# Kernel tuning notes

Measured on AMD Instinct MI355X. Metric: run time of the kernel, lower is better.

## Reference

```python
import jax, jax.numpy as jnp
import numpy as np

B, S, D, H = 32, 8192, 256, 256


def setup_inputs() -> dict:
    key = jax.random.key(0)
    ks = jax.random.split(key, 8)
    # start token: module uses np.random.seed(42); np.random.random([B,1,D])
    rng = np.random.RandomState(42)
    start_token = jnp.asarray(rng.random_sample((B, 1, D)).astype(np.float32))
    s = 0.05  # weight init scale
    return {
        "encoder_output": jax.random.normal(ks[0], (B, S, D), jnp.float32),
        "h0": jax.random.normal(ks[1], (B, H), jnp.float32),
        "c0": jax.random.normal(ks[2], (B, H), jnp.float32),
        "start_token": start_token,
        # Keras LSTM params: kernel [D,4H], recurrent_kernel [H,4H], bias [4H]; gate order i,f,c,o
        "W_k": jax.random.normal(ks[3], (D, 4 * H), jnp.float32) * s,
        "W_r": jax.random.normal(ks[4], (H, 4 * H), jnp.float32) * s,
        "b_lstm": jnp.zeros((4 * H,), jnp.float32),
        # encoder_weight Dense(H), decode_weight Dense(H), v Dense(1)
        "W_e": jax.random.normal(ks[5], (D, H), jnp.float32) * s,
        "b_e": jnp.zeros((H,), jnp.float32),
        "W_d": jax.random.normal(ks[6], (H, H), jnp.float32) * s,
        "b_d": jnp.zeros((H,), jnp.float32),
        "v_w": jax.random.normal(ks[7], (H, 1), jnp.float32) * s,
        "v_b": jnp.zeros((1,), jnp.float32),
    }


def reference(encoder_output, h0, c0, start_token, W_k, W_r, b_lstm,
              W_e, b_e, W_d, b_d, v_w, v_b):
    # --- one Keras-LSTM step on the start token (seq_len = 1) ---
    x = start_token[:, 0, :]                      # [B, D]
    z = x @ W_k + h0 @ W_r + b_lstm               # [B, 4H]
    i, f, g, o = jnp.split(z, 4, axis=-1)         # Keras gate order i,f,c,o
    c = jax.nn.sigmoid(f) * c0 + jax.nn.sigmoid(i) * jnp.tanh(g)
    h = jax.nn.sigmoid(o) * jnp.tanh(c)           # [B, H] decoder output
    # --- Bahdanau additive attention (vectorized form of the double loop) ---
    dec_proj = h @ W_d + b_d                      # [B, H]
    enc_proj = encoder_output @ W_e + b_e         # [B, S, H]
    # tanh(enc_proj + dec_proj) projected to scalar by v
    scores = jnp.tanh(enc_proj + dec_proj[:, None, :]) @ v_w  # [B, S, 1]
    scores = scores[..., 0] + v_b                 # [B, S]
    return jax.nn.softmax(scores, axis=-1)
```

## Files before the change

kernel.cpp:

```cpp
#include <hip/hip_runtime.h>
#include <hip/hip_bf16.h>
#include <stdint.h>

#define B 32
#define S 8192
#define D 256
#define H 256

typedef __attribute__((ext_vector_type(8))) short bf16x8;
typedef __attribute__((ext_vector_type(4))) float f32x4;

__device__ inline unsigned short f2bf(float f) {
  unsigned u = __float_as_uint(f);
  unsigned r = (u + 0x7FFFu + ((u >> 16) & 1u)) >> 16;
  return (unsigned short)r;
}

__device__ inline unsigned pk2bf(float a, float b) {
  __hip_bfloat162 h = __float22bfloat162_rn(make_float2(a, b));
  unsigned u;
  __builtin_memcpy(&u, &h, 4);
  return u;
}

__device__ inline bf16x8 pack8(float4 a, float4 b) {
  union { unsigned u[4]; bf16x8 v; } c;
  c.u[0] = pk2bf(a.x, a.y);
  c.u[1] = pk2bf(a.z, a.w);
  c.u[2] = pk2bf(b.x, b.y);
  c.u[3] = pk2bf(b.z, b.w);
  return c.v;
}

__device__ inline float fast_tanh(float x) {
  float e = __expf(2.0f * x);
  return 1.0f - 2.0f * __builtin_amdgcn_rcpf(1.0f + e);
}

__global__ __launch_bounds__(1024) void prep_kernel(
    const float* __restrict__ h0, const float* __restrict__ c0,
    const float* __restrict__ start_token, const float* __restrict__ W_k,
    const float* __restrict__ W_r, const float* __restrict__ b_lstm,
    const float* __restrict__ W_e, const float* __restrict__ W_d,
    const float* __restrict__ b_d,
    unsigned short* __restrict__ Wfrag, float* __restrict__ dec) {
  int blk = blockIdx.x;
  int tid = threadIdx.x;

  __shared__ float xs[D], hs[H], zs[4 * H], hv[H], dpp[4][H];

  if (blk < 64) {
    int gid = blk * 1024 + tid;
    int j = gid & 7;
    int lane = (gid >> 3) & 63;
    int kt = (gid >> 9) & 7;
    int nt = gid >> 12;
    int n = nt * 16 + (lane & 15);
    int k = kt * 32 + (lane >> 4) * 8 + j;
    Wfrag[gid] = f2bf(W_e[k * H + n]);
  } else {
    int b = blk - 64;
    if (tid < D) xs[tid] = start_token[b * D + tid];
    else if (tid < 2 * D) hs[tid - D] = h0[b * H + (tid - D)];
    __syncthreads();
    {
      int jj = tid;
      float a0 = 0.f, a1 = 0.f, a2 = 0.f, a3 = 0.f;
      #pragma unroll 8
      for (int d = 0; d < D; d += 4) {
        a0 += xs[d + 0] * W_k[(d + 0) * 1024 + jj];
        a1 += xs[d + 1] * W_k[(d + 1) * 1024 + jj];
        a2 += xs[d + 2] * W_k[(d + 2) * 1024 + jj];
        a3 += xs[d + 3] * W_k[(d + 3) * 1024 + jj];
      }
      #pragma unroll 8
      for (int h = 0; h < H; h += 4) {
        a0 += hs[h + 0] * W_r[(h + 0) * 1024 + jj];
        a1 += hs[h + 1] * W_r[(h + 1) * 1024 + jj];
        a2 += hs[h + 2] * W_r[(h + 2) * 1024 + jj];
        a3 += hs[h + 3] * W_r[(h + 3) * 1024 + jj];
      }
      zs[jj] = b_lstm[jj] + ((a0 + a1) + (a2 + a3));
    }
    __syncthreads();
    if (tid < H) {
      float zi = zs[tid], zf = zs[H + tid], zg = zs[2 * H + tid], zo = zs[3 * H + tid];
      float si = 1.0f / (1.0f + expf(-zi));
      float sf = 1.0f / (1.0f + expf(-zf));
      float so = 1.0f / (1.0f + expf(-zo));
      float c = sf * c0[b * H + tid] + si * tanhf(zg);
      hv[tid] = so * tanhf(c);
    }
    __syncthreads();
    {
      int hcol = tid & (H - 1);
      int q = tid >> 8;
      float a = 0.f;
      #pragma unroll 8
      for (int k = q * 64; k < q * 64 + 64; ++k) a += hv[k] * W_d[k * H + hcol];
      dpp[q][hcol] = a;
    }
    __syncthreads();
    if (tid < H)
      dec[b * H + tid] = dpp[0][tid] + dpp[1][tid] + dpp[2][tid] + dpp[3][tid] + b_d[tid];
  }
}

__global__ __launch_bounds__(256, 2) void attn_kernel(
    const float* __restrict__ enc, const unsigned short* __restrict__ Wfrag,
    const float* __restrict__ dec, const float* __restrict__ b_e,
    const float* __restrict__ v_w, float* __restrict__ scores) {
  __shared__ float part_sh[2][64];

  int tid = threadIdx.x;
  int b = blockIdx.x >> 7;
  int st = blockIdx.x & 127;
  long row0 = (long)b * S + st * 64;

  int wave = tid >> 6, lane = tid & 63;
  int ml = lane & 15, kg = lane >> 4;
  int wr = wave >> 1, wc = wave & 1;

  const float* arow0 = enc + (row0 + wr * 32 + ml) * (long)D + kg * 8;
  const float* arow1 = arow0 + 16 * D;

  float bs[8], vw8[8];
  #pragma unroll
  for (int q = 0; q < 8; ++q) {
    int n = wc * 128 + q * 16 + ml;
    bs[q] = b_e[n] + dec[b * H + n];
    vw8[q] = v_w[n];
  }

  f32x4 acc[2][8];
  #pragma unroll
  for (int i = 0; i < 2; ++i)
    #pragma unroll
    for (int q = 0; q < 8; ++q) acc[i][q] = (f32x4){0.f, 0.f, 0.f, 0.f};

  #pragma unroll
  for (int kt = 0; kt < 8; ++kt) {
    bf16x8 wfr[8];
    #pragma unroll
    for (int q = 0; q < 8; ++q) {
      const unsigned short* p = Wfrag + ((size_t)(((wc * 8 + q) * 8 + kt) * 64 + lane) << 3);
      wfr[q] = *(const bf16x8*)p;
    }
    float4 a0lo = *(const float4*)(arow0 + kt * 32);
    float4 a0hi = *(const float4*)(arow0 + kt * 32 + 4);
    float4 a1lo = *(const float4*)(arow1 + kt * 32);
    float4 a1hi = *(const float4*)(arow1 + kt * 32 + 4);
    bf16x8 afr0 = pack8(a0lo, a0hi);
    bf16x8 afr1 = pack8(a1lo, a1hi);
    #pragma unroll
    for (int q = 0; q < 8; ++q) {
      acc[0][q] = __builtin_amdgcn_mfma_f32_16x16x32_bf16(afr0, wfr[q], acc[0][q], 0, 0, 0);
      acc[1][q] = __builtin_amdgcn_mfma_f32_16x16x32_bf16(afr1, wfr[q], acc[1][q], 0, 0, 0);
    }
  }

  float part[8];
  #pragma unroll
  for (int v = 0; v < 8; ++v) part[v] = 0.f;
  #pragma unroll
  for (int q = 0; q < 8; ++q) {
    #pragma unroll
    for (int i = 0; i < 2; ++i)
      #pragma unroll
      for (int r = 0; r < 4; ++r)
        part[i * 4 + r] += fast_tanh(acc[i][q][r] + bs[q]) * vw8[q];
  }
  #pragma unroll
  for (int m = 1; m < 16; m <<= 1)
    #pragma unroll
    for (int v = 0; v < 8; ++v) part[v] += __shfl_xor(part[v], m, 64);
  if (ml == 0) {
    #pragma unroll
    for (int i = 0; i < 2; ++i)
      #pragma unroll
      for (int r = 0; r < 4; ++r)
        part_sh[wc][wr * 32 + i * 16 + kg * 4 + r] = part[i * 4 + r];
  }
  __syncthreads();
  if (tid < 64)
    scores[row0 + tid] = part_sh[0][tid] + part_sh[1][tid];
}

__global__ __launch_bounds__(1024) void softmax_kernel(
    const float* __restrict__ scores, float* __restrict__ out) {
  int b = blockIdx.x;
  int tid = threadIdx.x;
  __shared__ float red[16];
  const float* src = scores + (long)b * S;
  float v[8];
  float lmax = -1e30f;
  #pragma unroll
  for (int j = 0; j < 8; ++j) {
    v[j] = src[tid + j * 1024];
    lmax = fmaxf(lmax, v[j]);
  }
  #pragma unroll
  for (int m = 1; m < 64; m <<= 1) lmax = fmaxf(lmax, __shfl_xor(lmax, m, 64));
  if ((tid & 63) == 0) red[tid >> 6] = lmax;
  __syncthreads();
  float M = red[0];
  #pragma unroll
  for (int i = 1; i < 16; ++i) M = fmaxf(M, red[i]);
  __syncthreads();
  float ls = 0.f;
  #pragma unroll
  for (int j = 0; j < 8; ++j) {
    v[j] = __expf(v[j] - M);
    ls += v[j];
  }
  #pragma unroll
  for (int m = 1; m < 64; m <<= 1) ls += __shfl_xor(ls, m, 64);
  if ((tid & 63) == 0) red[tid >> 6] = ls;
  __syncthreads();
  float total = 0.f;
  #pragma unroll
  for (int i = 0; i < 16; ++i) total += red[i];
  float inv = __builtin_amdgcn_rcpf(total);
  #pragma unroll
  for (int j = 0; j < 8; ++j) out[(long)b * S + tid + j * 1024] = v[j] * inv;
}

extern "C" void kernel_launch(void* const* d_in, const int* in_sizes, int n_in,
                              void* d_out, int out_size, void* d_ws, size_t ws_size,
                              hipStream_t stream) {
  const float* enc         = (const float*)d_in[0];
  const float* h0          = (const float*)d_in[1];
  const float* c0          = (const float*)d_in[2];
  const float* start_token = (const float*)d_in[3];
  const float* W_k         = (const float*)d_in[4];
  const float* W_r         = (const float*)d_in[5];
  const float* b_lstm      = (const float*)d_in[6];
  const float* W_e         = (const float*)d_in[7];
  const float* b_e         = (const float*)d_in[8];
  const float* W_d         = (const float*)d_in[9];
  const float* b_d         = (const float*)d_in[10];
  const float* v_w         = (const float*)d_in[11];
  float* out = (float*)d_out;

  char* wsb = (char*)d_ws;
  float* scores         = (float*)wsb;
  unsigned short* Wfrag = (unsigned short*)(wsb + (size_t)B * S * 4);
  float* dec            = (float*)(wsb + (size_t)B * S * 4 + (size_t)D * H * 2);

  prep_kernel<<<96, 1024, 0, stream>>>(h0, c0, start_token, W_k, W_r, b_lstm,
                                       W_e, W_d, b_d, Wfrag, dec);
  attn_kernel<<<B * (S / 64), 256, 0, stream>>>(enc, Wfrag, dec, b_e, v_w, scores);
  softmax_kernel<<<B, 1024, 0, stream>>>(scores, out);
}
```

Measured before the change: 500.4 us.

## Persistent attention blocks with register-resident W_e and async LDS double buffering

The attention kernel changes from 4096 small blocks to 512 blocks that each loop over 16 tiles of 32 rows. Each wave keeps its 64-column slice of the bf16 W_e fragments in registers for the whole block instead of reloading it per tile. Encoder tiles are copied into swizzled, double-buffered LDS with global_load_lds, so the next tile's load overlaps the current tile's MFMA work. Each wave writes its own partial score and the softmax kernel sums the four, which quadruples the scores buffer and adds register pressure that may limit occupancy.

Result: faster. 433.8 us (-13.3%).

```diff
diff --git a/kernel.cpp b/kernel.cpp
--- a/kernel.cpp
+++ b/kernel.cpp
@@ -9,6 +9,9 @@
 
 typedef __attribute__((ext_vector_type(8))) short bf16x8;
 typedef __attribute__((ext_vector_type(4))) float f32x4;
+
+#define GLOBAL_AS __attribute__((address_space(1)))
+#define LDS_AS __attribute__((address_space(3)))
 
 __device__ inline unsigned short f2bf(float f) {
   unsigned u = __float_as_uint(f);
@@ -42,8 +45,8 @@
     const float* __restrict__ start_token, const float* __restrict__ W_k,
     const float* __restrict__ W_r, const float* __restrict__ b_lstm,
     const float* __restrict__ W_e, const float* __restrict__ W_d,
-    const float* __restrict__ b_d,
-    unsigned short* __restrict__ Wfrag, float* __restrict__ dec) {
+    const float* __restrict__ b_d, const float* __restrict__ b_e,
+    unsigned short* __restrict__ Wfrag, float* __restrict__ decb) {
   int blk = blockIdx.x;
   int tid = threadIdx.x;
 
@@ -102,101 +105,119 @@
     }
     __syncthreads();
     if (tid < H)
-      dec[b * H + tid] = dpp[0][tid] + dpp[1][tid] + dpp[2][tid] + dpp[3][tid] + b_d[tid];
+      decb[b * H + tid] = dpp[0][tid] + dpp[1][tid] + dpp[2][tid] + dpp[3][tid]
+                        + b_d[tid] + b_e[tid];
   }
 }
 
 __global__ __launch_bounds__(256, 2) void attn_kernel(
     const float* __restrict__ enc, const unsigned short* __restrict__ Wfrag,
-    const float* __restrict__ dec, const float* __restrict__ b_e,
-    const float* __restrict__ v_w, float* __restrict__ scores) {
-  __shared__ float part_sh[2][64];
-
-  int tid = threadIdx.x;
-  int b = blockIdx.x >> 7;
-  int st = blockIdx.x & 127;
-  long row0 = (long)b * S + st * 64;
-
-  int wave = tid >> 6, lane = tid & 63;
-  int ml = lane & 15, kg = lane >> 4;
-  int wr = wave >> 1, wc = wave & 1;
-
-  const float* arow0 = enc + (row0 + wr * 32 + ml) * (long)D + kg * 8;
-  const float* arow1 = arow0 + 16 * D;
-
-  float bs[8], vw8[8];
-  #pragma unroll
-  for (int q = 0; q < 8; ++q) {
-    int n = wc * 128 + q * 16 + ml;
-    bs[q] = b_e[n] + dec[b * H + n];
-    vw8[q] = v_w[n];
-  }
-
-  f32x4 acc[2][8];
-  #pragma unroll
-  for (int i = 0; i < 2; ++i)
-    #pragma unroll
-    for (int q = 0; q < 8; ++q) acc[i][q] = (f32x4){0.f, 0.f, 0.f, 0.f};
-
-  #pragma unroll
-  for (int kt = 0; kt < 8; ++kt) {
-    bf16x8 wfr[8];
-    #pragma unroll
-    for (int q = 0; q < 8; ++q) {
-      const unsigned short* p = Wfrag + ((size_t)(((wc * 8 + q) * 8 + kt) * 64 + lane) << 3);
-      wfr[q] = *(const bf16x8*)p;
-    }
-    float4 a0lo = *(const float4*)(arow0 + kt * 32);
-    float4 a0hi = *(const float4*)(arow0 + kt * 32 + 4);
-    float4 a1lo = *(const float4*)(arow1 + kt * 32);
-    float4 a1hi = *(const float4*)(arow1 + kt * 32 + 4);
-    bf16x8 afr0 = pack8(a0lo, a0hi);
-    bf16x8 afr1 = pack8(a1lo, a1hi);
-    #pragma unroll
-    for (int q = 0; q < 8; ++q) {
-      acc[0][q] = __builtin_amdgcn_mfma_f32_16x16x32_bf16(afr0, wfr[q], acc[0][q], 0, 0, 0);
-      acc[1][q] = __builtin_amdgcn_mfma_f32_16x16x32_bf16(afr1, wfr[q], acc[1][q], 0, 0, 0);
-    }
-  }
-
-  float part[8];
-  #pragma unroll
-  for (int v = 0; v < 8; ++v) part[v] = 0.f;
-  #pragma unroll
-  for (int q = 0; q < 8; ++q) {
+    const float* __restrict__ decb, const float* __restrict__ v_w,
+    float* __restrict__ scores4) {
+  __shared__ float Abuf[2][32 * 256];
+
+  const int tid = threadIdx.x;
+  const int wave = tid >> 6, lane = tid & 63;
+  const int ml = lane & 15, kg = lane >> 4;
+  const int bid = blockIdx.x;
+  const int batch = bid >> 4;
+  const long row_blk = (long)bid * 512;
+
+  bf16x8 wfr[4][8];
+  #pragma unroll
+  for (int q = 0; q < 4; ++q)
+    #pragma unroll
+    for (int kt = 0; kt < 8; ++kt)
+      wfr[q][kt] = *(const bf16x8*)(Wfrag + ((size_t)(((wave * 4 + q) * 8 + kt) * 64 + lane) << 3));
+
+  float bs[4], vw[4];
+  #pragma unroll
+  for (int q = 0; q < 4; ++q) {
+    int n = wave * 64 + q * 16 + ml;
+    bs[q] = decb[batch * 256 + n];
+    vw[q] = v_w[n];
+  }
+
+  auto stage = [&](int t, int sel) {
+    const float* gtile = enc + (row_blk + (long)t * 32) * D;
+    #pragma unroll
+    for (int is = 0; is < 8; ++is) {
+      int row = is * 4 + wave;
+      int c = lane ^ (row & 7);
+      const float* gp = gtile + row * D + c * 4;
+      float* lp = &Abuf[sel][(is * 256 + wave * 64) * 4];
+      __builtin_amdgcn_global_load_lds((const GLOBAL_AS void*)gp,
+                                       (LDS_AS void*)lp, 16, 0, 0);
+    }
+  };
+
+  stage(0, 0);
+
+  #pragma unroll 2
+  for (int t = 0; t < 16; ++t) {
+    __syncthreads();
+    if (t + 1 < 16) stage(t + 1, (t + 1) & 1);
+
+    const float* Ab = Abuf[t & 1];
+    f32x4 acc[2][4];
     #pragma unroll
     for (int i = 0; i < 2; ++i)
       #pragma unroll
-      for (int r = 0; r < 4; ++r)
-        part[i * 4 + r] += fast_tanh(acc[i][q][r] + bs[q]) * vw8[q];
-  }
-  #pragma unroll
-  for (int m = 1; m < 16; m <<= 1)
-    #pragma unroll
-    for (int v = 0; v < 8; ++v) part[v] += __shfl_xor(part[v], m, 64);
-  if (ml == 0) {
-    #pragma unroll
-    for (int i = 0; i < 2; ++i)
-      #pragma unroll
-      for (int r = 0; r < 4; ++r)
-        part_sh[wc][wr * 32 + i * 16 + kg * 4 + r] = part[i * 4 + r];
-  }
-  __syncthreads();
-  if (tid < 64)
-    scores[row0 + tid] = part_sh[0][tid] + part_sh[1][tid];
+      for (int q = 0; q < 4; ++q) acc[i][q] = (f32x4){0.f, 0.f, 0.f, 0.f};
+
+    #pragma unroll
+    for (int kt = 0; kt < 8; ++kt) {
+      #pragma unroll
+      for (int i = 0; i < 2; ++i) {
+        int row = i * 16 + ml;
+        int x = ml & 7;
+        int c0 = kt * 8 + kg * 2;
+        float4 v0 = *(const float4*)&Ab[(row * 64 + (c0 ^ x)) * 4];
+        float4 v1 = *(const float4*)&Ab[(row * 64 + ((c0 + 1) ^ x)) * 4];
+        bf16x8 af = pack8(v0, v1);
+        #pragma unroll
+        for (int q = 0; q < 4; ++q)
+          acc[i][q] = __builtin_amdgcn_mfma_f32_16x16x32_bf16(af, wfr[q][kt], acc[i][q], 0, 0, 0);
+      }
+    }
+
+    float part[8];
+    #pragma unroll
+    for (int v = 0; v < 8; ++v) part[v] = 0.f;
+    #pragma unroll
+    for (int q = 0; q < 4; ++q)
+      #pragma unroll
+      for (int i = 0; i < 2; ++i)
+        #pragma unroll
+        for (int r = 0; r < 4; ++r)
+          part[i * 4 + r] += fast_tanh(acc[i][q][r] + bs[q]) * vw[q];
+    #pragma unroll
+    for (int m = 1; m < 16; m <<= 1)
+      #pragma unroll
+      for (int v = 0; v < 8; ++v) part[v] += __shfl_xor(part[v], m, 64);
+    if (ml == 0) {
+      long r0 = row_blk + (long)t * 32 + kg * 4;
+      #pragma unroll
+      for (int i = 0; i < 2; ++i)
+        #pragma unroll
+        for (int r = 0; r < 4; ++r)
+          scores4[(r0 + i * 16 + r) * 4 + wave] = part[i * 4 + r];
+    }
+  }
 }
 
 __global__ __launch_bounds__(1024) void softmax_kernel(
-    const float* __restrict__ scores, float* __restrict__ out) {
+    const float* __restrict__ scores4, float* __restrict__ out) {
   int b = blockIdx.x;
   int tid = threadIdx.x;
   __shared__ float red[16];
-  const float* src = scores + (long)b * S;
+  const float* src = scores4 + (long)b * S * 4;
   float v[8];
   float lmax = -1e30f;
   #pragma unroll
   for (int j = 0; j < 8; ++j) {
-    v[j] = src[tid + j * 1024];
+    float4 t4 = *(const float4*)(src + (size_t)(tid + j * 1024) * 4);
+    v[j] = (t4.x + t4.y) + (t4.z + t4.w);
     lmax = fmaxf(lmax, v[j]);
   }
   #pragma unroll
@@ -243,12 +264,12 @@
   float* out = (float*)d_out;
 
   char* wsb = (char*)d_ws;
-  float* scores         = (float*)wsb;
-  unsigned short* Wfrag = (unsigned short*)(wsb + (size_t)B * S * 4);
-  float* dec            = (float*)(wsb + (size_t)B * S * 4 + (size_t)D * H * 2);
+  float* scores4        = (float*)wsb;
+  unsigned short* Wfrag = (unsigned short*)(wsb + (size_t)B * S * 16);
+  float* decb           = (float*)(wsb + (size_t)B * S * 16 + (size_t)D * H * 2);
 
   prep_kernel<<<96, 1024, 0, stream>>>(h0, c0, start_token, W_k, W_r, b_lstm,
-                                       W_e, W_d, b_d, Wfrag, dec);
-  attn_kernel<<<B * (S / 64), 256, 0, stream>>>(enc, Wfrag, dec, b_e, v_w, scores);
-  softmax_kernel<<<B, 1024, 0, stream>>>(scores, out);
-}
+                                       W_e, W_d, b_d, b_e, Wfrag, decb);
+  attn_kernel<<<512, 256, 0, stream>>>(enc, Wfrag, decb, v_w, scores4);
+  softmax_kernel<<<B, 1024, 0, stream>>>(scores4, out);
+}
```
